# Kernel optimization log

Measured on AMD Instinct MI355X. Metric: run time of the kernel, lower is better.

The kernel has to match this reference:

```python
import jax, jax.numpy as jnp
import numpy as np

C = 128
K = 7
RED = 4
C_RED = C // RED
PAD = (K - 1) // 2
BN_EPS = 1e-5


def setup_inputs() -> dict:
    key = jax.random.key(0)
    ks = jax.random.split(key, 7)
    b, h, w = 8, 56, 56
    x = jax.random.normal(ks[0], (b, C, h, w), dtype=jnp.float32)
    # 1x1 conv #1: c -> c_red
    w1 = jax.random.normal(ks[1], (C_RED, C), dtype=jnp.float32) * (1.0 / np.sqrt(C))
    b1 = jax.random.normal(ks[2], (C_RED,), dtype=jnp.float32) * 0.01
    # BatchNorm affine params
    gamma = jnp.ones((C_RED,), dtype=jnp.float32)
    beta = jnp.zeros((C_RED,), dtype=jnp.float32)
    # 1x1 conv #2: c_red -> k*k
    w2 = jax.random.normal(ks[3], (K * K, C_RED), dtype=jnp.float32) * (1.0 / np.sqrt(C_RED))
    b2 = jax.random.normal(ks[4], (K * K,), dtype=jnp.float32) * 0.01
    return {"x": x, "w1": w1, "b1": b1, "gamma": gamma, "beta": beta, "w2": w2, "b2": b2}


def _unfold(x):
    # torch.nn.Unfold(K, padding=PAD, stride=1) -> (b, c, k*k, h, w), channel-major
    b, c, h, w = x.shape
    xp = jnp.pad(x, ((0, 0), (0, 0), (PAD, PAD), (PAD, PAD)))
    patches = [xp[:, :, i:i + h, j:j + w] for i in range(K) for j in range(K)]
    return jnp.stack(patches, axis=2)  # (b, c, k*k, h, w)


def reference(x, w1, b1, gamma, beta, w2, b2):
    b, c, h, w = x.shape
    # kernel-generation branch: 1x1 conv -> BN (batch stats, training mode) -> ReLU -> 1x1 conv
    t = jnp.einsum('rc,bchw->brhw', w1, x) + b1[None, :, None, None]
    mean = t.mean(axis=(0, 2, 3))
    var = t.var(axis=(0, 2, 3))  # biased, as in torch BN normalization
    t = (t - mean[None, :, None, None]) * jax.lax.rsqrt(var + BN_EPS)[None, :, None, None]
    t = jax.nn.relu(t * gamma[None, :, None, None] + beta[None, :, None, None])
    kern = jnp.einsum('kr,brhw->bkhw', w2, t) + b2[None, :, None, None]  # (b, k*k, h, w)
    # involution: per-pixel kernel broadcast over channels, sum over k*k taps
    x_unf = _unfold(x)  # (b, c, k*k, h, w)
    return jnp.einsum('bkhw,bckhw->bchw', kern, x_unf)
```

## Files before the change

kernel.cpp:

```cpp
#include <hip/hip_runtime.h>

#define C 128
#define CRED 32
#define K 7
#define KK 49
#define H 56
#define W 56
#define P (H*W)
#define B 8
#define NPIX (B*P)
#define BN_EPS 1e-5

#define T_OFF 0
#define T_SIZE (B*CRED*P)
#define KERN_OFF (T_OFF + T_SIZE)
#define KERN_SIZE (B*KK*P)
#define NBLK_A (49*B)
#define PSUM_OFF (KERN_OFF + KERN_SIZE)
#define PSQ_OFF (PSUM_OFF + NBLK_A*CRED)
#define SS_OFF  (PSQ_OFF + NBLK_A*CRED)
#define SCALE_OFF SS_OFF
#define SHIFT_OFF (SS_OFF + CRED)
#define WS_NEED ((size_t)(SHIFT_OFF + CRED) * sizeof(float))

#define FB_SCALE_OFF T_SIZE
#define FB_SHIFT_OFF (T_SIZE + CRED)

__global__ __launch_bounds__(256) void kA_conv1(const float* __restrict__ x,
                                                const float* __restrict__ w1,
                                                const float* __restrict__ b1,
                                                float* __restrict__ ws) {
    int tid = threadIdx.x;
    int bx = blockIdx.x;
    int b  = blockIdx.y;
    int px = tid & 63;
    int p  = bx * 64 + px;
    int ru8 = __builtin_amdgcn_readfirstlane((tid >> 6) * 8);
    const float* __restrict__ wq = w1 + (size_t)ru8 * C;
    const float* xb = x + (size_t)b * C * P + p;

    float acc[8];
#pragma unroll
    for (int u = 0; u < 8; ++u) acc[u] = 0.f;
#pragma unroll 8
    for (int c = 0; c < C; ++c) {
        float xv = xb[(size_t)c * P];
#pragma unroll
        for (int u = 0; u < 8; ++u)
            acc[u] = fmaf(wq[u * C + c], xv, acc[u]);
    }
#pragma unroll
    for (int u = 0; u < 8; ++u) acc[u] += b1[ru8 + u];

    float* tb = ws + T_OFF + (size_t)b * CRED * P + p;
#pragma unroll
    for (int u = 0; u < 8; ++u)
        tb[(size_t)(ru8 + u) * P] = acc[u];

    float s[8], q[8];
#pragma unroll
    for (int u = 0; u < 8; ++u) { s[u] = acc[u]; q[u] = acc[u] * acc[u]; }
#pragma unroll
    for (int off = 32; off; off >>= 1) {
#pragma unroll
        for (int u = 0; u < 8; ++u) {
            s[u] += __shfl_xor(s[u], off);
            q[u] += __shfl_xor(q[u], off);
        }
    }
    if (px == 0) {
        int blk = b * 49 + bx;
        float* psum = ws + PSUM_OFF + (size_t)blk * CRED + ru8;
        float* psq  = ws + PSQ_OFF  + (size_t)blk * CRED + ru8;
#pragma unroll
        for (int u = 0; u < 8; ++u) { psum[u] = s[u]; psq[u] = q[u]; }
    }
}

__global__ __launch_bounds__(256) void kB_bnfin(const float* __restrict__ gamma,
                                                const float* __restrict__ beta,
                                                float* __restrict__ ws) {
    __shared__ double sd1[8][CRED];
    __shared__ double sd2[8][CRED];
    int tid = threadIdx.x;
    int r = tid & 31, g = tid >> 5;
    double s1 = 0.0, s2 = 0.0;
    for (int i = g * 49; i < g * 49 + 49; ++i) {
        s1 += (double)ws[PSUM_OFF + i * CRED + r];
        s2 += (double)ws[PSQ_OFF + i * CRED + r];
    }
    sd1[g][r] = s1; sd2[g][r] = s2;
    __syncthreads();
    if (tid < CRED) {
        double S1 = 0.0, S2 = 0.0;
        for (int gg = 0; gg < 8; ++gg) { S1 += sd1[gg][tid]; S2 += sd2[gg][tid]; }
        double mean = S1 / NPIX;
        double var = S2 / NPIX - mean * mean;
        double sc = (double)gamma[tid] / sqrt(var + BN_EPS);
        ws[SCALE_OFF + tid] = (float)sc;
        ws[SHIFT_OFF + tid] = (float)((double)beta[tid] - mean * sc);
    }
}

__global__ __launch_bounds__(256) void kC_kern(const float* __restrict__ w2,
                                               const float* __restrict__ b2,
                                               float* __restrict__ ws) {
    __shared__ float s_t[CRED * W];
    __shared__ float s_w2[KK * 33];
    int tid = threadIdx.x;
    int h = blockIdx.x, b = blockIdx.y;
    for (int i = tid; i < KK * CRED; i += 256) {
        int k = i >> 5, r = i & 31;
        s_w2[k * 33 + r] = w2[i];
    }
    const float* scale = ws + SCALE_OFF;
    const float* shift = ws + SHIFT_OFF;
    for (int i = tid; i < CRED * W; i += 256) {
        int r = i / W, w = i - r * W;
        float v = ws[T_OFF + ((size_t)b * CRED + r) * P + h * W + w];
        v = fmaf(v, scale[r], shift[r]);
        s_t[r * W + w] = fmaxf(v, 0.f);
    }
    __syncthreads();
    for (int i = tid; i < KK * 14; i += 256) {
        int k = i / 14, w0 = (i - k * 14) * 4;
        float bb = b2[k];
        float a0 = bb, a1 = bb, a2 = bb, a3 = bb;
#pragma unroll
        for (int r = 0; r < CRED; ++r) {
            float4 tv = *(const float4*)&s_t[r * W + w0];
            float wv = s_w2[k * 33 + r];
            a0 = fmaf(wv, tv.x, a0);
            a1 = fmaf(wv, tv.y, a1);
            a2 = fmaf(wv, tv.z, a2);
            a3 = fmaf(wv, tv.w, a3);
        }
        float4 o = {a0, a1, a2, a3};
        *(float4*)&ws[KERN_OFF + ((size_t)b * KK + k) * P + h * W + w0] = o;
    }
}

#define TH 8
#define XROWS 14
#define XPITCH 68
#define NG 4
__global__ __launch_bounds__(448) void kD3_inv(const float* __restrict__ x,
                                               const float* __restrict__ ws,
                                               float* __restrict__ out) {
    __shared__ float4 s_x[XROWS * NG * XPITCH];
    int tid = threadIdx.x;
    int bx = blockIdx.x;
    int z  = blockIdx.y;
    int b = bx / 7, ht = bx - b * 7;
    int h0 = ht * TH;
    int orow = tid / W;
    int ocol = tid - orow * W;

    int row0 = tid >> 6, col0 = tid & 63;
    int hh0 = h0 - 3 + row0, ww0 = col0 - 3;
    float m0 = ((unsigned)hh0 < H && (unsigned)ww0 < W) ? 1.f : 0.f;
    int off0 = (m0 != 0.f) ? (hh0 * W + ww0) : 0;
    int hh1 = hh0 + 7;
    float m1 = ((unsigned)hh1 < H && (unsigned)ww0 < W) ? 1.f : 0.f;
    int off1 = (m1 != 0.f) ? (hh1 * W + ww0) : 0;
    int slot0b = (row0 * NG) * XPITCH + col0;
    int slot1b = ((row0 + 7) * NG) * XPITCH + col0;

    int cg0 = z * 16;
    const size_t xbase = ((size_t)b * C + cg0) * P;

#pragma unroll
    for (int g = 0; g < NG; ++g) {
        const float* xc = x + xbase + (size_t)(4 * g) * P;
        float4 f0, f1;
        f0.x = xc[off0] * m0;          f0.y = xc[P + off0] * m0;
        f0.z = xc[2 * P + off0] * m0;  f0.w = xc[3 * P + off0] * m0;
        f1.x = xc[off1] * m1;          f1.y = xc[P + off1] * m1;
        f1.z = xc[2 * P + off1] * m1;  f1.w = xc[3 * P + off1] * m1;
        s_x[slot0b + g * XPITCH] = f0;
        s_x[slot1b + g * XPITCH] = f1;
    }
    __syncthreads();

    int p0 = h0 * W + tid;
    const float* kp = ws + KERN_OFF + (size_t)b * KK * P + p0;

    float4 acc[NG];
#pragma unroll
    for (int g = 0; g < NG; ++g) acc[g] = make_float4(0.f, 0.f, 0.f, 0.f);

    const float4* xs = s_x + orow * (NG * XPITCH) + ocol;
#pragma unroll 1
    for (int i = 0; i < K; ++i) {
        const float4* xr = xs + i * (NG * XPITCH);
#pragma unroll
        for (int j = 0; j < K; ++j) {
            float kv = kp[(size_t)(i * 7 + j) * P];
#pragma unroll
            for (int g = 0; g < NG; ++g) {
                float4 xv = xr[g * XPITCH + j];
                acc[g].x = fmaf(kv, xv.x, acc[g].x);
                acc[g].y = fmaf(kv, xv.y, acc[g].y);
                acc[g].z = fmaf(kv, xv.z, acc[g].z);
                acc[g].w = fmaf(kv, xv.w, acc[g].w);
            }
        }
    }

#pragma unroll
    for (int g = 0; g < NG; ++g) {
        float* ob = out + xbase + (size_t)(4 * g) * P + p0;
        ob[0]     = acc[g].x;
        ob[P]     = acc[g].y;
        ob[2 * P] = acc[g].z;
        ob[3 * P] = acc[g].w;
    }
}

__global__ __launch_bounds__(256) void k1_conv1(const float* __restrict__ x,
                                                const float* __restrict__ w1,
                                                const float* __restrict__ b1,
                                                float* __restrict__ t) {
    __shared__ float s_w1t[C * CRED];
    int tid = threadIdx.x;
    for (int i = tid; i < C * CRED; i += 256) {
        int c = i >> 5, r = i & 31;
        s_w1t[i] = w1[r * C + c];
    }
    __syncthreads();
    int b = blockIdx.y;
    int p = blockIdx.x * 256 + tid;
    if (p >= P) return;
    float acc[CRED];
#pragma unroll
    for (int r = 0; r < CRED; ++r) acc[r] = 0.f;
    const float* xb = x + (size_t)b * C * P + p;
    for (int c = 0; c < C; ++c) {
        float xv = xb[(size_t)c * P];
#pragma unroll
        for (int r = 0; r < CRED; ++r)
            acc[r] = fmaf(s_w1t[c * CRED + r], xv, acc[r]);
    }
    float* tb = t + (size_t)b * CRED * P + p;
#pragma unroll
    for (int r = 0; r < CRED; ++r)
        tb[(size_t)r * P] = acc[r] + b1[r];
}

__global__ __launch_bounds__(256) void k2_bnstats(const float* __restrict__ t,
                                                  const float* __restrict__ gamma,
                                                  const float* __restrict__ beta,
                                                  float* __restrict__ scale,
                                                  float* __restrict__ shift) {
    int r = blockIdx.x;
    int tid = threadIdx.x;
    double s = 0.0, s2 = 0.0;
    for (int i = tid; i < NPIX; i += 256) {
        int b = i / P, p = i - b * P;
        float v = t[((size_t)b * CRED + r) * P + p];
        s += v;
        s2 += (double)v * v;
    }
    __shared__ double ls[256], ls2[256];
    ls[tid] = s; ls2[tid] = s2;
    __syncthreads();
    for (int off = 128; off > 0; off >>= 1) {
        if (tid < off) { ls[tid] += ls[tid + off]; ls2[tid] += ls2[tid + off]; }
        __syncthreads();
    }
    if (tid == 0) {
        double mean = ls[0] / NPIX;
        double var = ls2[0] / NPIX - mean * mean;
        double sc = (double)gamma[r] / sqrt(var + BN_EPS);
        scale[r] = (float)sc;
        shift[r] = (float)((double)beta[r] - mean * sc);
    }
}

__global__ __launch_bounds__(256) void k3_involution(const float* __restrict__ x,
                                                     const float* __restrict__ t,
                                                     const float* __restrict__ scale,
                                                     const float* __restrict__ shift,
                                                     const float* __restrict__ w2,
                                                     const float* __restrict__ b2,
                                                     float* __restrict__ out) {
    int h = blockIdx.x;
    int b = blockIdx.y;
    int z = blockIdx.z;
    int tid = threadIdx.x;
    __shared__ float s_w2[KK * CRED];
    __shared__ float s_t[CRED * W];
    __shared__ float s_kern[KK][W];
    __shared__ float s_x[4][K][64];
    for (int i = tid; i < KK * CRED; i += 256) s_w2[i] = w2[i];
    for (int i = tid; i < CRED * W; i += 256) {
        int r = i / W, w = i - r * W;
        float v = t[((size_t)b * CRED + r) * P + h * W + w];
        v = fmaf(v, scale[r], shift[r]);
        s_t[r * W + w] = fmaxf(v, 0.f);
    }
    __syncthreads();
    for (int i = tid; i < KK * W; i += 256) {
        int k = i / W, w = i - k * W;
        float acc = b2[k];
#pragma unroll
        for (int r = 0; r < CRED; ++r)
            acc = fmaf(s_w2[k * CRED + r], s_t[r * W + w], acc);
        s_kern[k][w] = acc;
    }
    __syncthreads();
    int w = tid % W;
    int c4 = tid / W;
    float kr[KK];
#pragma unroll
    for (int k = 0; k < KK; ++k) kr[k] = s_kern[k][w];
    int cbase = z * (C / 2);
    for (int cg = cbase; cg < cbase + C / 2; cg += 4) {
        for (int i = tid; i < 4 * K * 64; i += 256) {
            int col = i & 63;
            int rc = i >> 6;
            int cc = rc / K;
            int row = rc - cc * K;
            int hh = h - 3 + row;
            int ww = col - 3;
            float v = 0.f;
            if ((unsigned)hh < H && (unsigned)ww < W)
                v = x[(((size_t)b * C + cg + cc) * H + hh) * W + ww];
            s_x[cc][row][col] = v;
        }
        __syncthreads();
        if (tid < 4 * W) {
            float acc = 0.f;
#pragma unroll
            for (int i = 0; i < K; ++i)
#pragma unroll
                for (int j = 0; j < K; ++j)
                    acc = fmaf(kr[i * K + j], s_x[c4][i][w + j], acc);
            out[(((size_t)b * C + cg + c4) * H + h) * W + w] = acc;
        }
        __syncthreads();
    }
}

extern "C" void kernel_launch(void* const* d_in, const int* in_sizes, int n_in,
                              void* d_out, int out_size, void* d_ws, size_t ws_size,
                              hipStream_t stream) {
    const float* x     = (const float*)d_in[0];
    const float* w1    = (const float*)d_in[1];
    const float* b1    = (const float*)d_in[2];
    const float* gamma = (const float*)d_in[3];
    const float* beta  = (const float*)d_in[4];
    const float* w2    = (const float*)d_in[5];
    const float* b2    = (const float*)d_in[6];
    float* out = (float*)d_out;
    float* ws  = (float*)d_ws;

    if (ws_size >= WS_NEED) {
        dim3 gA(49, B);
        kA_conv1<<<gA, 256, 0, stream>>>(x, w1, b1, ws);
        kB_bnfin<<<1, 256, 0, stream>>>(gamma, beta, ws);
        dim3 gC(H, B);
        kC_kern<<<gC, 256, 0, stream>>>(w2, b2, ws);
        dim3 gD(7 * B, 8);
        kD3_inv<<<gD, 448, 0, stream>>>(x, ws, out);
    } else {
        float* t     = ws;
        float* scale = ws + FB_SCALE_OFF;
        float* shift = ws + FB_SHIFT_OFF;
        dim3 g1((P + 255) / 256, B);
        k1_conv1<<<g1, 256, 0, stream>>>(x, w1, b1, t);
        k2_bnstats<<<CRED, 256, 0, stream>>>(t, gamma, beta, scale, shift);
        dim3 g3(H, B, 2);
        k3_involution<<<g3, 256, 0, stream>>>(x, t, scale, shift, w2, b2, out);
    }
}
```

Measured before the change: 47.64 us.

## Retile involution kernel to compute two output rows per thread with vertical x reuse

Replaces the involution kernel with one that gives each thread two vertically adjacent output rows and 8 channels instead of one row and 16 channels. Each staged x row in shared memory is reused for both rows' kernel taps, so shared-memory reads per FMA drop. The tile grows to 14 rows with 20 halo rows and the grid is flattened to 512 blocks with batch in the low bits. The cost is that 56 of 448 threads sit idle during compute, and the loop runs 8 masked row iterations.

```diff
diff --git a/kernel.cpp b/kernel.cpp
--- a/kernel.cpp
+++ b/kernel.cpp
@@ -140,80 +140,95 @@
     }
 }
 
-#define TH 8
-#define XROWS 14
-#define XPITCH 68
-#define NG 4
-__global__ __launch_bounds__(448) void kD3_inv(const float* __restrict__ x,
+#define TH4 14
+#define XR4 20
+#define XP4 68
+#define NG4 2
+__global__ __launch_bounds__(448) void kD4_inv(const float* __restrict__ x,
                                                const float* __restrict__ ws,
                                                float* __restrict__ out) {
-    __shared__ float4 s_x[XROWS * NG * XPITCH];
-    int tid = threadIdx.x;
-    int bx = blockIdx.x;
-    int z  = blockIdx.y;
-    int b = bx / 7, ht = bx - b * 7;
-    int h0 = ht * TH;
-    int orow = tid / W;
-    int ocol = tid - orow * W;
-
-    int row0 = tid >> 6, col0 = tid & 63;
-    int hh0 = h0 - 3 + row0, ww0 = col0 - 3;
-    float m0 = ((unsigned)hh0 < H && (unsigned)ww0 < W) ? 1.f : 0.f;
-    int off0 = (m0 != 0.f) ? (hh0 * W + ww0) : 0;
-    int hh1 = hh0 + 7;
-    float m1 = ((unsigned)hh1 < H && (unsigned)ww0 < W) ? 1.f : 0.f;
-    int off1 = (m1 != 0.f) ? (hh1 * W + ww0) : 0;
-    int slot0b = (row0 * NG) * XPITCH + col0;
-    int slot1b = ((row0 + 7) * NG) * XPITCH + col0;
-
-    int cg0 = z * 16;
+    __shared__ float4 s_x[XR4 * NG4 * XP4];
+    int tid = threadIdx.x;
+    int bid = blockIdx.x;
+    int b    = bid & 7;
+    int z    = (bid >> 3) & 15;
+    int tile = bid >> 7;
+    int h0 = tile * TH4;
+    int rp = tid / W;
+    int c  = tid - rp * W;
+    bool owns = rp < 7;
+    int r0 = h0 + 2 * rp;
+
+    int cg0 = z * (4 * NG4);
     const size_t xbase = ((size_t)b * C + cg0) * P;
 
 #pragma unroll
-    for (int g = 0; g < NG; ++g) {
-        const float* xc = x + xbase + (size_t)(4 * g) * P;
-        float4 f0, f1;
-        f0.x = xc[off0] * m0;          f0.y = xc[P + off0] * m0;
-        f0.z = xc[2 * P + off0] * m0;  f0.w = xc[3 * P + off0] * m0;
-        f1.x = xc[off1] * m1;          f1.y = xc[P + off1] * m1;
-        f1.z = xc[2 * P + off1] * m1;  f1.w = xc[3 * P + off1] * m1;
-        s_x[slot0b + g * XPITCH] = f0;
-        s_x[slot1b + g * XPITCH] = f1;
-    }
-    __syncthreads();
-
-    int p0 = h0 * W + tid;
-    const float* kp = ws + KERN_OFF + (size_t)b * KK * P + p0;
-
-    float4 acc[NG];
-#pragma unroll
-    for (int g = 0; g < NG; ++g) acc[g] = make_float4(0.f, 0.f, 0.f, 0.f);
-
-    const float4* xs = s_x + orow * (NG * XPITCH) + ocol;
+    for (int s = 0; s < 6; ++s) {
+        int lin = tid + s * 448;
+        if (lin < XR4 * NG4 * 64) {
+            int row = lin >> 7;
+            int rem = lin & 127;
+            int g   = rem >> 6;
+            int col = rem & 63;
+            int hh = h0 - 3 + row, ww = col - 3;
+            float m = ((unsigned)hh < H && (unsigned)ww < W) ? 1.f : 0.f;
+            int off = (m != 0.f) ? (hh * W + ww) : 0;
+            const float* xc = x + xbase + (size_t)(4 * g) * P;
+            float4 f;
+            f.x = xc[off] * m;          f.y = xc[P + off] * m;
+            f.z = xc[2 * P + off] * m;  f.w = xc[3 * P + off] * m;
+            s_x[(row * NG4 + g) * XP4 + col] = f;
+        }
+    }
+    __syncthreads();
+
+    int p0 = owns ? (r0 * W + c) : 0;
+    const float* kp0 = ws + KERN_OFF + (size_t)b * KK * P + p0;
+    const float* kp1 = kp0 + W;
+
+    float4 a00 = make_float4(0,0,0,0), a01 = a00;
+    float4 a10 = a00, a11 = a00;
+
+    const float4* xs = s_x + (2 * rp * NG4) * XP4 + c;
+
+    float kv0[7], kv1[7];
 #pragma unroll 1
-    for (int i = 0; i < K; ++i) {
-        const float4* xr = xs + i * (NG * XPITCH);
-#pragma unroll
-        for (int j = 0; j < K; ++j) {
-            float kv = kp[(size_t)(i * 7 + j) * P];
-#pragma unroll
-            for (int g = 0; g < NG; ++g) {
-                float4 xv = xr[g * XPITCH + j];
-                acc[g].x = fmaf(kv, xv.x, acc[g].x);
-                acc[g].y = fmaf(kv, xv.y, acc[g].y);
-                acc[g].z = fmaf(kv, xv.z, acc[g].z);
-                acc[g].w = fmaf(kv, xv.w, acc[g].w);
-            }
-        }
-    }
-
-#pragma unroll
-    for (int g = 0; g < NG; ++g) {
-        float* ob = out + xbase + (size_t)(4 * g) * P + p0;
-        ob[0]     = acc[g].x;
-        ob[P]     = acc[g].y;
-        ob[2 * P] = acc[g].z;
-        ob[3 * P] = acc[g].w;
+    for (int ri = 0; ri < 8; ++ri) {
+        float mk0 = (ri <= 6) ? 1.f : 0.f;
+        float mk1 = (ri >= 1) ? 1.f : 0.f;
+        int t0 = ((ri <= 6) ? ri : 6) * 7;
+        int t1 = ((ri >= 1) ? ri - 1 : 0) * 7;
+#pragma unroll
+        for (int j = 0; j < 7; ++j) kv0[j] = kp0[(size_t)(t0 + j) * P] * mk0;
+#pragma unroll
+        for (int j = 0; j < 7; ++j) kv1[j] = kp1[(size_t)(t1 + j) * P] * mk1;
+
+        const float4* xr = xs + ri * (NG4 * XP4);
+#pragma unroll
+        for (int j = 0; j < 7; ++j) {
+            float4 xv0 = xr[j];
+            float4 xv1 = xr[XP4 + j];
+            float k0 = kv0[j], k1 = kv1[j];
+            a00.x = fmaf(k0, xv0.x, a00.x);  a00.y = fmaf(k0, xv0.y, a00.y);
+            a00.z = fmaf(k0, xv0.z, a00.z);  a00.w = fmaf(k0, xv0.w, a00.w);
+            a10.x = fmaf(k1, xv0.x, a10.x);  a10.y = fmaf(k1, xv0.y, a10.y);
+            a10.z = fmaf(k1, xv0.z, a10.z);  a10.w = fmaf(k1, xv0.w, a10.w);
+            a01.x = fmaf(k0, xv1.x, a01.x);  a01.y = fmaf(k0, xv1.y, a01.y);
+            a01.z = fmaf(k0, xv1.z, a01.z);  a01.w = fmaf(k0, xv1.w, a01.w);
+            a11.x = fmaf(k1, xv1.x, a11.x);  a11.y = fmaf(k1, xv1.y, a11.y);
+            a11.z = fmaf(k1, xv1.z, a11.z);  a11.w = fmaf(k1, xv1.w, a11.w);
+        }
+    }
+
+    if (owns) {
+        float* o0 = out + xbase + p0;
+        float* o1 = o0 + W;
+        o0[0] = a00.x;  o0[P] = a00.y;  o0[2*P] = a00.z;  o0[3*P] = a00.w;
+        o1[0] = a10.x;  o1[P] = a10.y;  o1[2*P] = a10.z;  o1[3*P] = a10.w;
+        float* o2 = o0 + 4 * P;
+        float* o3 = o1 + 4 * P;
+        o2[0] = a01.x;  o2[P] = a01.y;  o2[2*P] = a01.z;  o2[3*P] = a01.w;
+        o3[0] = a11.x;  o3[P] = a11.y;  o3[2*P] = a11.z;  o3[3*P] = a11.w;
     }
 }
 
@@ -361,8 +376,7 @@
         kB_bnfin<<<1, 256, 0, stream>>>(gamma, beta, ws);
         dim3 gC(H, B);
         kC_kern<<<gC, 256, 0, stream>>>(w2, b2, ws);
-        dim3 gD(7 * B, 8);
-        kD3_inv<<<gD, 448, 0, stream>>>(x, ws, out);
+        kD4_inv<<<512, 448, 0, stream>>>(x, ws, out);
     } else {
         float* t     = ws;
         float* scale = ws + FB_SCALE_OFF;
```

Result: faster. 46.05 us (-3.3%).
